# Optimization experiments

Hardware: AMD Instinct MI355X
Metric: run time of the kernel (lower is better)

Reference implementation:

```python
import jax, jax.numpy as jnp
import numpy as np

N_SUPPORT = 65536
N_QUERY = 65536
FEAT = 1024
EMBED = 512
WAYS = 256


def setup_inputs() -> dict:
    key = jax.random.key(0)
    k1, k2, k3, k4 = jax.random.split(key, 4)
    support_images = jax.random.normal(k1, (N_SUPPORT, FEAT), dtype=jnp.float32)
    query_images = jax.random.normal(k2, (N_QUERY, FEAT), dtype=jnp.float32)
    # deterministic labels so every one of the `ways` classes is non-empty
    labels = jnp.arange(N_SUPPORT, dtype=jnp.int32) % WAYS
    support_labels = jax.nn.one_hot(labels, WAYS, dtype=jnp.int32)  # one-hot, as in torch forward
    W = jax.random.normal(k3, (FEAT, EMBED), dtype=jnp.float32) / np.sqrt(FEAT).astype(np.float32)
    b = jax.random.normal(k4, (EMBED,), dtype=jnp.float32) * 0.01
    return {
        "support_images": support_images,
        "support_labels": support_labels,
        "query_images": query_images,
        "W": W,
        "b": b,
    }


def reference(support_images, support_labels, query_images, W, b):
    ways = support_labels.shape[1]
    labels = jnp.argmax(support_labels, axis=1)  # [N_support]

    # backbone: Linear(feat -> embed)
    z_support = support_images @ W + b  # [N_support, E]
    z_query = query_images @ W + b      # [N_query, E]

    # fused per-class mean (replaces the python loop over classes)
    sums = jax.ops.segment_sum(z_support, labels, num_segments=ways)          # [ways, E]
    counts = jax.ops.segment_sum(jnp.ones((z_support.shape[0],), z_support.dtype),
                                 labels, num_segments=ways)                   # [ways]
    z_proto = sums / counts[:, None]

    # scores = -cdist(z_query, z_proto)  (euclidean, p=2)
    q2 = jnp.sum(z_query * z_query, axis=1, keepdims=True)   # [Nq, 1]
    p2 = jnp.sum(z_proto * z_proto, axis=1)[None, :]          # [1, ways]
    d2 = q2 + p2 - 2.0 * (z_query @ z_proto.T)                # [Nq, ways]
    scores = -jnp.sqrt(jnp.maximum(d2, 0.0))

    return jax.nn.softmax(scores, axis=1)
```

## Files before the change

### kernel.cpp

```cpp
#include <hip/hip_runtime.h>
#include <stdint.h>

#define NSUP 65536
#define NQRY 65536
#define FEAT 1024
#define EMB  512
#define WAYS 256

typedef unsigned short u16;
typedef unsigned int   u32;
typedef __attribute__((ext_vector_type(8))) __bf16 bf16x8;
typedef __attribute__((ext_vector_type(4))) float  f32x4;

static __device__ __forceinline__ u16 f2bf(float f) {
    u32 u = __builtin_bit_cast(u32, f);
    u32 r = u + 0x7fffu + ((u >> 16) & 1u);
    return (u16)(r >> 16);
}

static __device__ __forceinline__ void gl_lds16(const void* g, void* l) {
    __builtin_amdgcn_global_load_lds((const __attribute__((address_space(1))) u32*)g,
                                     (__attribute__((address_space(3))) u32*)l,
                                     16, 0, 0);
}

static __device__ __forceinline__ int swz16(int r, int s) {
    return r * 32 + ((s ^ ((r >> 1) & 3)) * 8);
}

__global__ __launch_bounds__(256) void k0_transpose(const float* __restrict__ W,
                                                    u16* __restrict__ Wt,
                                                    int* __restrict__ icounts) {
    const int t = threadIdx.x;
    if (blockIdx.x == 0) icounts[t] = 0;
    __shared__ float tile[64][65];
    const int bx = blockIdx.x;
    const int k0 = (bx & 15) * 64;
    const int e0 = (bx >> 4) * 64;
#pragma unroll
    for (int i = 0; i < 16; ++i) {
        int idx = t + i * 256;
        int kk = idx >> 6, ee = idx & 63;
        tile[kk][ee] = W[(size_t)(k0 + kk) * EMB + e0 + ee];
    }
    __syncthreads();
#pragma unroll
    for (int i = 0; i < 16; ++i) {
        int idx = t + i * 256;
        int ee = idx >> 6, kk = idx & 63;
        Wt[(size_t)(e0 + ee) * FEAT + k0 + kk] = f2bf(tile[kk][ee]);
    }
}

__global__ __launch_bounds__(256) void k1a_labels(const int* __restrict__ sl,
                                                  int* __restrict__ labels,
                                                  int* __restrict__ icounts) {
    const int row = blockIdx.x * 4 + (threadIdx.x >> 6);
    const int lane = threadIdx.x & 63;
    const int4* p = (const int4*)(sl + (size_t)row * WAYS);
    int4 v = p[lane];
    int my = -1;
    if (v.x) my = lane * 4 + 0;
    if (v.y) my = lane * 4 + 1;
    if (v.z) my = lane * 4 + 2;
    if (v.w) my = lane * 4 + 3;
#pragma unroll
    for (int m = 32; m; m >>= 1) my = max(my, __shfl_xor(my, m));
    if (lane == 0) {
        labels[row] = my;
        atomicAdd(&icounts[my], 1);
    }
}

__global__ __launch_bounds__(256) void k1p_prefix(const int* __restrict__ icounts,
                                                  int* __restrict__ offs,
                                                  int* __restrict__ cursor,
                                                  float* __restrict__ countsF) {
    __shared__ int s[256];
    const int t = threadIdx.x;
    const int v = icounts[t];
    s[t] = v;
    __syncthreads();
    for (int d = 1; d < 256; d <<= 1) {
        int x = (t >= d) ? s[t - d] : 0;
        __syncthreads();
        s[t] += x;
        __syncthreads();
    }
    const int exc = s[t] - v;
    offs[t] = exc;
    cursor[t] = exc;
    countsF[t] = (float)v;
}

__global__ __launch_bounds__(256) void k1s_scatter(const int* __restrict__ labels,
                                                   int* __restrict__ cursor,
                                                   int* __restrict__ perm) {
    const int r = blockIdx.x * 256 + threadIdx.x;
    const int lb = labels[r];
    const int pos = atomicAdd(&cursor[lb], 1);
    perm[pos] = r;
}

__global__ __launch_bounds__(512) void k2_proto(const float* __restrict__ sums,
                                                const float* __restrict__ counts,
                                                const float* __restrict__ W,
                                                u16* __restrict__ zpb,
                                                float* __restrict__ p2) {
    __shared__ float proto[FEAT];
    __shared__ float red[8];
    const int c = blockIdx.x, t = threadIdx.x;
    const float inv = 1.0f / counts[c];
    proto[t]       = sums[(size_t)c * FEAT + t] * inv;
    proto[t + 512] = sums[(size_t)c * FEAT + t + 512] * inv;
    __syncthreads();
    float a0 = 0.f, a1 = 0.f, a2 = 0.f, a3 = 0.f;
#pragma unroll 8
    for (int k = 0; k < FEAT; k += 4) {
        a0 += proto[k + 0] * W[(size_t)(k + 0) * EMB + t];
        a1 += proto[k + 1] * W[(size_t)(k + 1) * EMB + t];
        a2 += proto[k + 2] * W[(size_t)(k + 2) * EMB + t];
        a3 += proto[k + 3] * W[(size_t)(k + 3) * EMB + t];
    }
    float z = (a0 + a1) + (a2 + a3);
    zpb[(size_t)c * EMB + t] = f2bf(z);
    float sq = z * z;
#pragma unroll
    for (int m = 1; m < 64; m <<= 1) sq += __shfl_xor(sq, m);
    if ((t & 63) == 0) red[t >> 6] = sq;
    __syncthreads();
    if (t == 0) {
        float s = 0.f;
#pragma unroll
        for (int i = 0; i < 8; ++i) s += red[i];
        p2[c] = s;
    }
}

__global__ __launch_bounds__(1024, 4) void k13_fused(const float* __restrict__ Q,
                                                     const u16* __restrict__ Wt,
                                                     u16* __restrict__ zq,
                                                     float* __restrict__ q2,
                                                     const float* __restrict__ img,
                                                     const int* __restrict__ perm,
                                                     const int* __restrict__ offs,
                                                     const int* __restrict__ icounts,
                                                     float* __restrict__ sums) {
    const int bx = blockIdx.x;
    const int t = threadIdx.x;

    if (bx % 3 == 2) {
        const int c = bx / 3;
        const int base = offs[c];
        const int n    = icounts[c];
        float acc = 0.f;
        int i = 0;
        for (; i + 8 <= n; i += 8) {
            int rr[8];
#pragma unroll
            for (int u = 0; u < 8; ++u) rr[u] = perm[base + i + u];
            float v[8];
#pragma unroll
            for (int u = 0; u < 8; ++u) v[u] = img[(size_t)rr[u] * FEAT + t];
#pragma unroll
            for (int u = 0; u < 8; ++u) acc += v[u];
        }
        for (; i < n; ++i) acc += img[(size_t)perm[base + i] * FEAT + t];
        sums[(size_t)c * FEAT + t] = acc;
        return;
    }

    const int kb = (bx / 3) * 2 + (bx % 3);
    __shared__ u16 Asl[2][128 * 32];
    __shared__ u16 Bsl[2][512 * 32];
    const int lane = t & 63, wave = t >> 6;
    const int wm = wave >> 3, wn = wave & 7;
    const int L = lane & 15, g = lane >> 4;
    const size_t row0 = (size_t)kb * 128;

    const int ar = t >> 2, as = t & 3;
    const float* aptr = Q + (row0 + ar) * FEAT + as * 8;
    const int aw = swz16(ar, as);
    float af[8];

    auto loadA = [&](int ks) {
        const float4* p = (const float4*)(aptr + ks * 32);
        float4 x = p[0], y = p[1];
        af[0] = x.x; af[1] = x.y; af[2] = x.z; af[3] = x.w;
        af[4] = y.x; af[5] = y.y; af[6] = y.z; af[7] = y.w;
    };
    auto writeA = [&](int buf) {
        uint4 w;
        w.x = (u32)f2bf(af[0]) | ((u32)f2bf(af[1]) << 16);
        w.y = (u32)f2bf(af[2]) | ((u32)f2bf(af[3]) << 16);
        w.z = (u32)f2bf(af[4]) | ((u32)f2bf(af[5]) << 16);
        w.w = (u32)f2bf(af[6]) | ((u32)f2bf(af[7]) << 16);
        *(uint4*)&Asl[buf][aw] = w;
    };
    auto stageB = [&](int buf, int ks) {
#pragma unroll
        for (int p = 0; p < 2; ++p) {
            int gi = t + p * 1024;
            int r = gi >> 2, cc = gi & 3;
            int s = cc ^ ((r >> 1) & 3);
            gl_lds16(Wt + (size_t)r * FEAT + ks * 32 + s * 8, &Bsl[buf][gi * 8]);
        }
    };

    f32x4 acc[4][4];
#pragma unroll
    for (int mt = 0; mt < 4; ++mt)
#pragma unroll
        for (int nt = 0; nt < 4; ++nt) acc[mt][nt] = f32x4{0.f, 0.f, 0.f, 0.f};

    stageB(0, 0);
    if (t < 512) { loadA(0); writeA(0); }
    __syncthreads();

    const int ard = swz16(wm * 64 + L, g);
    const int brd = swz16(wn * 64 + L, g);

    int cur = 0;
    for (int ks = 0; ks < 32; ++ks) {
        const int nxt = cur ^ 1;
        if (ks < 31) {
            stageB(nxt, ks + 1);
            if (t < 512) loadA(ks + 1);
        }
        bf16x8 a[4], b[4];
#pragma unroll
        for (int mt = 0; mt < 4; ++mt) a[mt] = *(const bf16x8*)&Asl[cur][ard + mt * 512];
#pragma unroll
        for (int nt = 0; nt < 4; ++nt) b[nt] = *(const bf16x8*)&Bsl[cur][brd + nt * 512];
#pragma unroll
        for (int mt = 0; mt < 4; ++mt)
#pragma unroll
            for (int nt = 0; nt < 4; ++nt)
                acc[mt][nt] = __builtin_amdgcn_mfma_f32_16x16x32_bf16(a[mt], b[nt], acc[mt][nt], 0, 0, 0);
        if (ks < 31 && t < 512) writeA(nxt);
        __syncthreads();
        cur = nxt;
    }

    float* q2part = (float*)&Asl[0][0];
    const int c = L;
#pragma unroll
    for (int mt = 0; mt < 4; ++mt) {
#pragma unroll
        for (int j = 0; j < 4; ++j) {
            const int rloc = wm * 64 + mt * 16 + g * 4 + j;
            const size_t r = row0 + rloc;
            float ss = 0.f;
#pragma unroll
            for (int nt = 0; nt < 4; ++nt) {
                float v = acc[mt][nt][j];
                ss += v * v;
                zq[r * EMB + wn * 64 + nt * 16 + c] = f2bf(v);
            }
#pragma unroll
            for (int m = 1; m < 16; m <<= 1) ss += __shfl_xor(ss, m);
            if (c == 0) q2part[wn * 128 + rloc] = ss;
        }
    }
    __syncthreads();
    if (t < 128) {
        float s0 = 0.f;
#pragma unroll
        for (int p = 0; p < 8; ++p) s0 += q2part[p * 128 + t];
        q2[row0 + t] = s0;
    }
}

__global__ __launch_bounds__(256, 2) void k4_scores(const u16* __restrict__ zq,
                                                    const u16* __restrict__ zp,
                                                    const float* __restrict__ q2,
                                                    const float* __restrict__ p2,
                                                    float* __restrict__ out) {
    __shared__ u16 zps[16][32 * 32];
    const int t = threadIdx.x;
    const int lane = t & 63, wave = t >> 6;
    const int L = lane & 15, g = lane >> 4;
    const size_t row0 = (size_t)blockIdx.x * 64 + wave * 16;

    bf16x8 a[16];
    const u16* arow = zq + (row0 + L) * EMB + g * 8;
#pragma unroll
    for (int ks = 0; ks < 16; ++ks) a[ks] = *(const bf16x8*)(arow + ks * 32);

    float q2v[4];
#pragma unroll
    for (int j = 0; j < 4; ++j) q2v[j] = q2[row0 + g * 4 + j];
    float p2v[16];
#pragma unroll
    for (int i = 0; i < 16; ++i) p2v[i] = p2[i * 16 + L];

    f32x4 acc[16];
#pragma unroll
    for (int i = 0; i < 16; ++i) acc[i] = f32x4{0.f, 0.f, 0.f, 0.f};

    for (int c = 0; c < 8; ++c) {
        if (c) __syncthreads();
#pragma unroll
        for (int p = 0; p < 8; ++p) {
            int gi = t + p * 256;
            int kc = gi >> 7, way = (gi >> 2) & 31, slot = gi & 3;
            int s = slot ^ ((way >> 1) & 3);
            gl_lds16(zp + (size_t)(c * 32 + way) * EMB + kc * 32 + s * 8,
                     ((u16*)zps) + gi * 8);
        }
        asm volatile("s_waitcnt vmcnt(0)" ::: "memory");
        __syncthreads();
#pragma unroll
        for (int ks = 0; ks < 16; ++ks) {
#pragma unroll
            for (int nt = 0; nt < 2; ++nt) {
                bf16x8 b = *(const bf16x8*)&zps[ks][swz16(nt * 16 + L, g)];
                acc[c * 2 + nt] = __builtin_amdgcn_mfma_f32_16x16x32_bf16(a[ks], b, acc[c * 2 + nt], 0, 0, 0);
            }
        }
    }

    float mx[4] = {-1e30f, -1e30f, -1e30f, -1e30f};
#pragma unroll
    for (int i = 0; i < 16; ++i)
#pragma unroll
        for (int j = 0; j < 4; ++j) {
            float d2 = q2v[j] + p2v[i] - 2.f * acc[i][j];
            float s = -sqrtf(fmaxf(d2, 0.f));
            acc[i][j] = s;
            mx[j] = fmaxf(mx[j], s);
        }
#pragma unroll
    for (int j = 0; j < 4; ++j)
#pragma unroll
        for (int m = 1; m < 16; m <<= 1) mx[j] = fmaxf(mx[j], __shfl_xor(mx[j], m));

    float sm[4] = {0.f, 0.f, 0.f, 0.f};
#pragma unroll
    for (int i = 0; i < 16; ++i)
#pragma unroll
        for (int j = 0; j < 4; ++j) {
            float e = __expf(acc[i][j] - mx[j]);
            acc[i][j] = e;
            sm[j] += e;
        }
#pragma unroll
    for (int j = 0; j < 4; ++j) {
#pragma unroll
        for (int m = 1; m < 16; m <<= 1) sm[j] += __shfl_xor(sm[j], m);
        sm[j] = 1.f / sm[j];
    }
#pragma unroll
    for (int i = 0; i < 16; ++i)
#pragma unroll
        for (int j = 0; j < 4; ++j)
            out[(row0 + g * 4 + j) * WAYS + i * 16 + L] = acc[i][j] * sm[j];
}

extern "C" void kernel_launch(void* const* d_in, const int* in_sizes, int n_in,
                              void* d_out, int out_size, void* d_ws, size_t ws_size,
                              hipStream_t stream) {
    (void)in_sizes; (void)n_in; (void)out_size; (void)ws_size;
    const float* simg = (const float*)d_in[0];
    const int*   slab = (const int*)d_in[1];
    const float* qimg = (const float*)d_in[2];
    const float* W    = (const float*)d_in[3];
    float* out = (float*)d_out;
    char* ws = (char*)d_ws;

    int*   labels = (int*)  (ws + 0);
    int*   perm   = (int*)  (ws + 262144);
    int*   icounts= (int*)  (ws + 524288);
    int*   offs   = (int*)  (ws + 525312);
    int*   cursor = (int*)  (ws + 526336);
    float* countsF= (float*)(ws + 527360);
    float* sums   = (float*)(ws + 528384);
    float* p2     = (float*)(ws + 1576960);
    u16*   zpb    = (u16*)  (ws + 1577984);
    u16*   Wt     = (u16*)  (ws + 1840128);
    u16*   zq     = (u16*)  (ws + 2888704);
    float* q2     = (float*)(ws + 69997568);


    k0_transpose <<<128,        256, 0, stream>>>(W, Wt, icounts);
    k1a_labels   <<<NSUP / 4,   256, 0, stream>>>(slab, labels, icounts);
    k1p_prefix   <<<1,          256, 0, stream>>>(icounts, offs, cursor, countsF);
    k1s_scatter  <<<NSUP / 256, 256, 0, stream>>>(labels, cursor, perm);
    k13_fused    <<<768,        1024, 0, stream>>>(qimg, Wt, zq, q2,
                                                   simg, perm, offs, icounts, sums);
    k2_proto     <<<WAYS,       512, 0, stream>>>(sums, countsF, W, zpb, p2);
    k4_scores    <<<NQRY / 64,  256, 0, stream>>>(zq, zpb, q2, p2, out);
}
```

Measured before the change: 348.1 us.

## Triple-buffer query GEMM with manual waitcnt pipelining and all-thread A loads

Turns the double-buffered query projection GEMM into a three-slot ring that keeps two K-steps of loads in flight. Barriers become raw s_barrier with explicit vmcnt/lgkmcnt waits instead of __syncthreads. The A-tile fp32 load is now spread over all 1024 threads (one float4 each) instead of 512 threads loading 8 floats. The extra LDS slot costs occupancy headroom, and the hand-counted waitcnt values must match the exact number of outstanding loads or the results are wrong.

```diff
diff --git a/kernel.cpp b/kernel.cpp
--- a/kernel.cpp
+++ b/kernel.cpp
@@ -22,6 +22,10 @@
     __builtin_amdgcn_global_load_lds((const __attribute__((address_space(1))) u32*)g,
                                      (__attribute__((address_space(3))) u32*)l,
                                      16, 0, 0);
+}
+
+static __device__ __forceinline__ void barrier_fenced() {
+    asm volatile("s_barrier" ::: "memory");
 }
 
 static __device__ __forceinline__ int swz16(int r, int s) {
@@ -171,39 +175,32 @@
     }
 
     const int kb = (bx / 3) * 2 + (bx % 3);
-    __shared__ u16 Asl[2][128 * 32];
-    __shared__ u16 Bsl[2][512 * 32];
+    __shared__ u16 Asl[3][128 * 32];
+    __shared__ u16 Bsl[3][512 * 32];
     const int lane = t & 63, wave = t >> 6;
     const int wm = wave >> 3, wn = wave & 7;
     const int L = lane & 15, g = lane >> 4;
     const size_t row0 = (size_t)kb * 128;
 
-    const int ar = t >> 2, as = t & 3;
-    const float* aptr = Q + (row0 + ar) * FEAT + as * 8;
-    const int aw = swz16(ar, as);
-    float af[8];
-
-    auto loadA = [&](int ks) {
-        const float4* p = (const float4*)(aptr + ks * 32);
-        float4 x = p[0], y = p[1];
-        af[0] = x.x; af[1] = x.y; af[2] = x.z; af[3] = x.w;
-        af[4] = y.x; af[5] = y.y; af[6] = y.z; af[7] = y.w;
+    const float* aptr = Q + (row0 + (t >> 3)) * FEAT + (t & 7) * 4;
+    const int aw = swz16(t >> 3, (t & 7) >> 1) + (t & 1) * 4;
+
+    auto loadA = [&](int ks, float4& af) {
+        af = *(const float4*)(aptr + ks * 32);
     };
-    auto writeA = [&](int buf) {
-        uint4 w;
-        w.x = (u32)f2bf(af[0]) | ((u32)f2bf(af[1]) << 16);
-        w.y = (u32)f2bf(af[2]) | ((u32)f2bf(af[3]) << 16);
-        w.z = (u32)f2bf(af[4]) | ((u32)f2bf(af[5]) << 16);
-        w.w = (u32)f2bf(af[6]) | ((u32)f2bf(af[7]) << 16);
-        *(uint4*)&Asl[buf][aw] = w;
+    auto writeA = [&](int slot, const float4& af) {
+        uint2 w;
+        w.x = (u32)f2bf(af.x) | ((u32)f2bf(af.y) << 16);
+        w.y = (u32)f2bf(af.z) | ((u32)f2bf(af.w) << 16);
+        *(uint2*)&Asl[slot][aw] = w;
     };
-    auto stageB = [&](int buf, int ks) {
+    auto stageB = [&](int slot, int ks) {
 #pragma unroll
         for (int p = 0; p < 2; ++p) {
             int gi = t + p * 1024;
             int r = gi >> 2, cc = gi & 3;
             int s = cc ^ ((r >> 1) & 3);
-            gl_lds16(Wt + (size_t)r * FEAT + ks * 32 + s * 8, &Bsl[buf][gi * 8]);
+            gl_lds16(Wt + (size_t)r * FEAT + ks * 32 + s * 8, &Bsl[slot][gi * 8]);
         }
     };
 
@@ -212,36 +209,63 @@
     for (int mt = 0; mt < 4; ++mt)
 #pragma unroll
         for (int nt = 0; nt < 4; ++nt) acc[mt][nt] = f32x4{0.f, 0.f, 0.f, 0.f};
-
-    stageB(0, 0);
-    if (t < 512) { loadA(0); writeA(0); }
-    __syncthreads();
 
     const int ard = swz16(wm * 64 + L, g);
     const int brd = swz16(wn * 64 + L, g);
 
-    int cur = 0;
-    for (int ks = 0; ks < 32; ++ks) {
-        const int nxt = cur ^ 1;
-        if (ks < 31) {
-            stageB(nxt, ks + 1);
-            if (t < 512) loadA(ks + 1);
-        }
+    auto compute = [&](int slot) {
         bf16x8 a[4], b[4];
 #pragma unroll
-        for (int mt = 0; mt < 4; ++mt) a[mt] = *(const bf16x8*)&Asl[cur][ard + mt * 512];
-#pragma unroll
-        for (int nt = 0; nt < 4; ++nt) b[nt] = *(const bf16x8*)&Bsl[cur][brd + nt * 512];
+        for (int mt = 0; mt < 4; ++mt) a[mt] = *(const bf16x8*)&Asl[slot][ard + mt * 512];
+#pragma unroll
+        for (int nt = 0; nt < 4; ++nt) b[nt] = *(const bf16x8*)&Bsl[slot][brd + nt * 512];
 #pragma unroll
         for (int mt = 0; mt < 4; ++mt)
 #pragma unroll
             for (int nt = 0; nt < 4; ++nt)
                 acc[mt][nt] = __builtin_amdgcn_mfma_f32_16x16x32_bf16(a[mt], b[nt], acc[mt][nt], 0, 0, 0);
-        if (ks < 31 && t < 512) writeA(nxt);
-        __syncthreads();
-        cur = nxt;
-    }
-
+    };
+
+    float4 afA, afB;
+    loadA(0, afA); stageB(0, 0);
+    loadA(1, afB); stageB(1, 1);
+    asm volatile("s_waitcnt vmcnt(5)" ::: "memory");
+    writeA(0, afA);
+    asm volatile("s_waitcnt vmcnt(3)" ::: "memory");
+    asm volatile("s_waitcnt lgkmcnt(0)" ::: "memory");
+    barrier_fenced();
+
+    for (int tt = 0; tt < 30; tt += 2) {
+        {
+            loadA(tt + 2, afA); stageB((tt + 2) % 3, tt + 2);
+            compute(tt % 3);
+            asm volatile("s_waitcnt vmcnt(5)" ::: "memory");
+            writeA((tt + 1) % 3, afB);
+            asm volatile("s_waitcnt vmcnt(3)" ::: "memory");
+            asm volatile("s_waitcnt lgkmcnt(0)" ::: "memory");
+            barrier_fenced();
+        }
+        {
+            loadA(tt + 3, afB); stageB((tt + 3) % 3, tt + 3);
+            compute((tt + 1) % 3);
+            asm volatile("s_waitcnt vmcnt(5)" ::: "memory");
+            writeA((tt + 2) % 3, afA);
+            asm volatile("s_waitcnt vmcnt(3)" ::: "memory");
+            asm volatile("s_waitcnt lgkmcnt(0)" ::: "memory");
+            barrier_fenced();
+        }
+    }
+    {
+        compute(0);
+        asm volatile("s_waitcnt vmcnt(2)" ::: "memory");
+        writeA(1, afB);
+        asm volatile("s_waitcnt vmcnt(0)" ::: "memory");
+        asm volatile("s_waitcnt lgkmcnt(0)" ::: "memory");
+        barrier_fenced();
+    }
+    compute(1);
+
+    __syncthreads();
     float* q2part = (float*)&Asl[0][0];
     const int c = L;
 #pragma unroll
```

Measured after the change: 341.9 us. Within noise of the previous version (-1.8%).
